# Kernel tuning notes

Measured on AMD Instinct MI355X. Metric: run time of the kernel, lower is better.

The kernel has to match this reference:

```python
import jax, jax.numpy as jnp
import numpy as np

INPUT_DIM = 1024
HIDDEN_DIM = 2048
LATENT_DIM = 256
NUM_EMBEDDINGS = 8192
COMMITMENT_COST = 0.25
BATCH = 16384


def setup_inputs() -> dict:
    key = jax.random.key(0)
    ks = jax.random.split(key, 10)
    def lin(k, fan_in, fan_out):
        # torch nn.Linear default init: U(-1/sqrt(fan_in), 1/sqrt(fan_in))
        bound = 1.0 / np.sqrt(fan_in)
        kw, kb = jax.random.split(k)
        W = jax.random.uniform(kw, (fan_in, fan_out), jnp.float32, -bound, bound)
        b = jax.random.uniform(kb, (fan_out,), jnp.float32, -bound, bound)
        return W, b
    enc_w1, enc_b1 = lin(ks[0], INPUT_DIM, HIDDEN_DIM)
    enc_w2, enc_b2 = lin(ks[1], HIDDEN_DIM, LATENT_DIM)
    dec_w1, dec_b1 = lin(ks[2], LATENT_DIM, HIDDEN_DIM)
    dec_w2, dec_b2 = lin(ks[3], HIDDEN_DIM, INPUT_DIM)
    # codebook init: U(-1/K, 1/K)
    codebook = jax.random.uniform(ks[4], (NUM_EMBEDDINGS, LATENT_DIM), jnp.float32,
                                  -1.0 / NUM_EMBEDDINGS, 1.0 / NUM_EMBEDDINGS)
    x = jax.random.uniform(ks[5], (BATCH, INPUT_DIM), jnp.float32)
    return {"x": x,
            "enc_w1": enc_w1, "enc_b1": enc_b1, "enc_w2": enc_w2, "enc_b2": enc_b2,
            "codebook": codebook,
            "dec_w1": dec_w1, "dec_b1": dec_b1, "dec_w2": dec_w2, "dec_b2": dec_b2}


def reference(x, enc_w1, enc_b1, enc_w2, enc_b2, codebook,
              dec_w1, dec_b1, dec_w2, dec_b2):
    # Encoder: relu(x W1 + b1) W2 + b2 -> z [N, latent]
    h = jax.nn.relu(x @ enc_w1 + enc_b1)
    z = h @ enc_w2 + enc_b2

    # Vector quantizer: squared-L2 distances to codebook [N, K]
    d = (jnp.sum(z * z, axis=1, keepdims=True)
         + jnp.sum(codebook * codebook, axis=1)
         - 2.0 * (z @ codebook.T))
    idx = jnp.argmin(d, axis=1)          # [N] int
    z_q = codebook[idx]                   # gather [N, latent]

    vq_loss = jnp.mean((jax.lax.stop_gradient(z_q) - z) ** 2)
    commit_loss = COMMITMENT_COST * jnp.mean((z_q - jax.lax.stop_gradient(z)) ** 2)
    loss = vq_loss + commit_loss

    # straight-through estimator
    z_q = z + jax.lax.stop_gradient(z_q - z)

    # Decoder: sigmoid(relu(z_q Wd1 + bd1) Wd2 + bd2)
    hd = jax.nn.relu(z_q @ dec_w1 + dec_b1)
    x_recon = jax.nn.sigmoid(hd @ dec_w2 + dec_b2)
    return (x_recon, loss)
```

## Files before the change

### kernel.cpp

```cpp
#include <hip/hip_runtime.h>
#include <math.h>

typedef unsigned short u16;
typedef __bf16 bf16x8 __attribute__((ext_vector_type(8)));
typedef float  f32x4  __attribute__((ext_vector_type(4)));

constexpr int B_  = 16384;
constexpr int DIN = 1024;
constexpr int DH  = 2048;
constexpr int DL  = 256;
constexpr int NE  = 8192;

__device__ __forceinline__ u16 f2bf(float f) {
    union { float f; unsigned u; } v; v.f = f;
    unsigned r = v.u + 0x7fffu + ((v.u >> 16) & 1u);
    return (u16)(r >> 16);
}
__device__ __forceinline__ float bf2f(u16 h) {
    union { unsigned u; float f; } v; v.u = ((unsigned)h) << 16;
    return v.f;
}

#define GLD16(gp, lp)                                                  \
    __builtin_amdgcn_global_load_lds(                                  \
        (__attribute__((address_space(1))) void*)(gp),                 \
        (__attribute__((address_space(3))) void*)(lp), 16, 0, 0)

#define SCHED0() __builtin_amdgcn_sched_barrier(0)
#define BARRIER() do { SCHED0(); __builtin_amdgcn_s_barrier(); SCHED0(); } while (0)
#define WAITV0() asm volatile("s_waitcnt vmcnt(0)" ::: "memory")
#define WAITV3() asm volatile("s_waitcnt vmcnt(3)" ::: "memory")

__device__ __forceinline__ void dev_cast(const float* __restrict__ in,
                                         u16* __restrict__ out, long blk)
{
    const size_t i = ((size_t)blk * 256 + threadIdx.x) * 4;
    float4 v = *(const float4*)(in + i);
    ushort4 o;
    o.x = f2bf(v.x); o.y = f2bf(v.y); o.z = f2bf(v.z); o.w = f2bf(v.w);
    *(ushort4*)(out + i) = o;
}

__device__ __forceinline__ void dev_transpose(const float* __restrict__ in,
                                              u16* __restrict__ out,
                                              int R, int C, long bx, long by,
                                              float (*t)[33])
{
    const int tx = threadIdx.x & 31, ty = threadIdx.x >> 5;
#pragma unroll
    for (int p = 0; p < 4; ++p)
        t[ty + p * 8][tx] = in[(by * 32 + ty + p * 8) * (long)C + bx * 32 + tx];
    __syncthreads();
#pragma unroll
    for (int p = 0; p < 4; ++p)
        out[(bx * 32 + ty + p * 8) * (long)R + by * 32 + tx] = f2bf(t[tx][ty + p * 8]);
}

__global__ __launch_bounds__(256)
void prep_fused(const float* __restrict__ x,   u16* __restrict__ x_bf,
                const float* __restrict__ cb,  u16* __restrict__ cb_bf,
                const float* __restrict__ ew1, u16* __restrict__ w1t,
                const float* __restrict__ ew2, u16* __restrict__ w2t,
                const float* __restrict__ dw1, u16* __restrict__ wd1t,
                const float* __restrict__ dw2, u16* __restrict__ wd2t,
                float* __restrict__ cn2)
{
    __shared__ float t[32][33];
    const long b = blockIdx.x;

    if (b < 16384) {
        dev_cast(x, x_bf, b);
    } else if (b < 18432) {
        dev_cast(cb, cb_bf, b - 16384);
    } else if (b < 20480) {
        const long r = b - 18432;
        dev_transpose(ew1, w1t, DIN, DH, r % 64, r / 64, t);
    } else if (b < 20992) {
        const long r = b - 20480;
        dev_transpose(ew2, w2t, DH, DL, r % 8, r / 8, t);
    } else if (b < 21504) {
        const long r = b - 20992;
        dev_transpose(dw1, wd1t, DL, DH, r % 64, r / 64, t);
    } else if (b < 23552) {
        const long r = b - 21504;
        dev_transpose(dw2, wd2t, DH, DIN, r % 32, r / 32, t);
    } else {
        const long r = b - 23552;
        const int code = (int)((r * 256 + threadIdx.x) >> 6);
        const int lane = threadIdx.x & 63;
        float4 v = *(const float4*)(cb + (long)code * DL + lane * 4);
        float s = fmaf(v.x, v.x, fmaf(v.y, v.y, fmaf(v.z, v.z, v.w * v.w)));
#pragma unroll
        for (int off = 32; off; off >>= 1) s += __shfl_down(s, off);
        if (lane == 0) cn2[code] = 0.5f * s;
    }
}

template <int EPI>
__global__ __launch_bounds__(512, 4)
void gemm_big_bf16(const u16* __restrict__ A, const u16* __restrict__ Bt,
                   const float* __restrict__ bias, void* __restrict__ Cout,
                   int M, int N, int K)
{
    __shared__ __align__(16) u16 As[3 * 8192];
    __shared__ __align__(16) u16 Bs[3 * 4096];

    const int tid = threadIdx.x;
    const int w = tid >> 6, l = tid & 63;
    const int wm = w >> 1, wn = w & 1;

    const int nbx   = N >> 7;
    const int nwg   = (M >> 8) * nbx;
    const int chunk = nwg >> 3;
    const int wg    = ((int)blockIdx.x & 7) * chunk + ((int)blockIdx.x >> 3);
    const long by   = wg / nbx;
    const long bx   = wg % nbx;

    const int lr  = l >> 2;
    const int lsw = (l & 3) ^ ((l >> 3) & 3);
    const int lg  = l >> 4, lm = l & 15;
    const int sx  = (lm >> 1) & 3;

    const u16* Abase = A  + (size_t)(by * 256) * K;
    const u16* Bbase = Bt + (size_t)(bx * 128) * K;

    f32x4 acc[4][4] = {};

    auto stage = [&](int k0, int b) {
        u16* dA = As + b * 8192;
        u16* dB = Bs + b * 4096;
#pragma unroll
        for (int i = 0; i < 2; ++i) {
            const int seg = w * 2 + i;
            GLD16(Abase + (size_t)(seg * 16 + lr) * K + k0 + lsw * 8,
                  dA + seg * 512);
        }
        GLD16(Bbase + (size_t)(w * 16 + lr) * K + k0 + lsw * 8,
              dB + w * 512);
    };

    const int NT = K >> 5;
    stage(0, 0);
    stage(32, 1);

    int cur = 0, pre = 2;
    for (int t = 0; t < NT; ++t) {
        if (t + 1 < NT) { WAITV3(); } else { WAITV0(); }
        BARRIER();
        if (t + 2 < NT) stage((t + 2) << 5, pre);

        const u16* as = As + cur * 8192;
        const u16* bs = Bs + cur * 4096;
        bf16x8 af[4], bfr[4];
#pragma unroll
        for (int m = 0; m < 4; ++m) {
            const int R = wm * 64 + m * 16 + lm;
            af[m] = *(const bf16x8*)&as[R * 32 + ((lg ^ sx) * 8)];
        }
#pragma unroll
        for (int n = 0; n < 4; ++n) {
            const int R = wn * 64 + n * 16 + lm;
            bfr[n] = *(const bf16x8*)&bs[R * 32 + ((lg ^ sx) * 8)];
        }
#pragma unroll
        for (int m = 0; m < 4; ++m)
#pragma unroll
            for (int n = 0; n < 4; ++n)
                acc[m][n] = __builtin_amdgcn_mfma_f32_16x16x32_bf16(
                    af[m], bfr[n], acc[m][n], 0, 0, 0);

        cur = (cur == 2) ? 0 : cur + 1;
        pre = (pre == 2) ? 0 : pre + 1;
    }

#pragma unroll
    for (int n = 0; n < 4; ++n) {
        const long col = bx * 128 + wn * 64 + n * 16 + lm;
        const float bb = bias[col];
#pragma unroll
        for (int m = 0; m < 4; ++m) {
#pragma unroll
            for (int j = 0; j < 4; ++j) {
                const long row = by * 256 + wm * 64 + m * 16 + lg * 4 + j;
                float e = acc[m][n][j] + bb;
                if (EPI == 1) e = fmaxf(e, 0.f);
                if (EPI == 2) {
                    e = 1.f / (1.f + expf(-e));
                    ((float*)Cout)[row * (long)N + col] = e;
                } else {
                    ((u16*)Cout)[row * (long)N + col] = f2bf(e);
                }
            }
        }
    }
}

template <int EPI>
__global__ __launch_bounds__(256, 4)
void gemm_64_bf16(const u16* __restrict__ A, const u16* __restrict__ Bt,
                  const float* __restrict__ bias, void* __restrict__ Cout,
                  int M, int N, int K)
{
    __shared__ __align__(16) u16 As[3 * 2048];
    __shared__ __align__(16) u16 Bs[3 * 4096];

    const int tid = threadIdx.x;
    const int w = tid >> 6, l = tid & 63;

    const int nbx   = N >> 7;
    const int nwg   = (M >> 6) * nbx;
    const int chunk = nwg >> 3;
    const int wg    = ((int)blockIdx.x & 7) * chunk + ((int)blockIdx.x >> 3);
    const long by   = wg / nbx;
    const long bx   = wg % nbx;

    const int lr  = l >> 2;
    const int lsw = (l & 3) ^ ((l >> 3) & 3);
    const int lg  = l >> 4, lm = l & 15;
    const int sx  = (lm >> 1) & 3;

    const u16* Abase = A  + (size_t)(by * 64) * K;
    const u16* Bbase = Bt + (size_t)(bx * 128) * K;

    f32x4 acc[4][2] = {};

    auto stage = [&](int k0, int b) {
        u16* dA = As + b * 2048;
        u16* dB = Bs + b * 4096;
        GLD16(Abase + (size_t)(w * 16 + lr) * K + k0 + lsw * 8, dA + w * 512);
#pragma unroll
        for (int i = 0; i < 2; ++i) {
            const int seg = w * 2 + i;
            GLD16(Bbase + (size_t)(seg * 16 + lr) * K + k0 + lsw * 8,
                  dB + seg * 512);
        }
    };

    const int NT = K >> 5;
    stage(0, 0);
    stage(32, 1);

    int cur = 0, pre = 2;
    for (int t = 0; t < NT; ++t) {
        if (t + 1 < NT) { WAITV3(); } else { WAITV0(); }
        BARRIER();
        if (t + 2 < NT) stage((t + 2) << 5, pre);

        const u16* as = As + cur * 2048;
        const u16* bs = Bs + cur * 4096;
        bf16x8 af[4], bfr[2];
#pragma unroll
        for (int m = 0; m < 4; ++m)
            af[m] = *(const bf16x8*)&as[(m * 16 + lm) * 32 + ((lg ^ sx) * 8)];
#pragma unroll
        for (int n = 0; n < 2; ++n) {
            const int R = w * 32 + n * 16 + lm;
            bfr[n] = *(const bf16x8*)&bs[R * 32 + ((lg ^ sx) * 8)];
        }
#pragma unroll
        for (int m = 0; m < 4; ++m)
#pragma unroll
            for (int n = 0; n < 2; ++n)
                acc[m][n] = __builtin_amdgcn_mfma_f32_16x16x32_bf16(
                    af[m], bfr[n], acc[m][n], 0, 0, 0);

        cur = (cur == 2) ? 0 : cur + 1;
        pre = (pre == 2) ? 0 : pre + 1;
    }

#pragma unroll
    for (int n = 0; n < 2; ++n) {
        const long col = bx * 128 + w * 32 + n * 16 + lm;
        const float bb = bias[col];
#pragma unroll
        for (int m = 0; m < 4; ++m) {
#pragma unroll
            for (int j = 0; j < 4; ++j) {
                const long row = by * 64 + m * 16 + lg * 4 + j;
                float e = acc[m][n][j] + bb;
                if (EPI == 2) {
                    e = 1.f / (1.f + expf(-e));
                    ((float*)Cout)[row * (long)N + col] = e;
                } else {
                    ((u16*)Cout)[row * (long)N + col] = f2bf(e);
                }
            }
        }
    }
}

__global__ __launch_bounds__(256, 2)
void vq_score2(const u16* __restrict__ z, const u16* __restrict__ cbt,
               const float* __restrict__ cn2,
               float* __restrict__ val8, int* __restrict__ idx8)
{
    __shared__ __align__(16) u16 lds[32768];

    const int tid = threadIdx.x;
    const int w = tid >> 6, l = tid & 63;
    const int rq = blockIdx.x >> 3;
    const int q  = blockIdx.x & 7;

    const int st_row8 = tid >> 5;
    const int st_s    = (tid & 31) ^ st_row8;
    const int lg = l >> 4, lm = l & 15;
    const int swz_x = l & 7;

    bf16x8 af[4][8];
    const long zbase_row = (long)rq * 256;
#pragma unroll
    for (int h = 0; h < 2; ++h) {
#pragma unroll
        for (int i = 0; i < 16; ++i) {
            const int row = i * 8 + st_row8;
            const u16* g = z + (zbase_row + h * 128 + row) * DL + st_s * 8;
            GLD16(g, lds + ((size_t)i * 256 + w * 64) * 8);
        }
        __syncthreads();
        if ((w >> 1) == h) {
            const int lrow0 = (w & 1) * 64;
#pragma unroll
            for (int m = 0; m < 4; ++m) {
                const int lrow = lrow0 + m * 16 + lm;
#pragma unroll
                for (int kg = 0; kg < 8; ++kg) {
                    const int s = (kg * 4 + lg) ^ swz_x;
                    af[m][kg] = *(const bf16x8*)&lds[lrow * 256 + s * 8];
                }
            }
        }
        __syncthreads();
    }

    const int code00 = q * (NE / 8);

    float bestv[16];
    int   besti[16];
#pragma unroll
    for (int k = 0; k < 16; ++k) { bestv[k] = 1e30f; besti[k] = 0; }

    auto stage_tile = [&](int t) {
        const int b = t & 1;
#pragma unroll
        for (int i = 0; i < 8; ++i) {
            const int c = i * 8 + st_row8;
            const u16* g = cbt + (size_t)(code00 + t * 64 + c) * DL + st_s * 8;
            GLD16(g, lds + ((size_t)b * 16384 + ((size_t)i * 256 + w * 64) * 8));
        }
    };

    stage_tile(0);
    __syncthreads();

    for (int t = 0; t < 16; ++t) {
        if (t < 15) stage_tile(t + 1);
        const u16* buf = lds + (size_t)(t & 1) * 16384;

#pragma unroll
        for (int n = 0; n < 4; ++n) {
            const int code_g = code00 + t * 64 + n * 16 + lm;
            const float cn2v = cn2[code_g];
            bf16x8 bfr[8];
#pragma unroll
            for (int kg = 0; kg < 8; ++kg) {
                const int lrow = n * 16 + lm;
                const int s = (kg * 4 + lg) ^ swz_x;
                bfr[kg] = *(const bf16x8*)&buf[lrow * 256 + s * 8];
            }
            f32x4 acc[4] = {};
#pragma unroll
            for (int kg = 0; kg < 8; ++kg)
#pragma unroll
                for (int m = 0; m < 4; ++m)
                    acc[m] = __builtin_amdgcn_mfma_f32_16x16x32_bf16(
                        af[m][kg], bfr[kg], acc[m], 0, 0, 0);
#pragma unroll
            for (int m = 0; m < 4; ++m)
#pragma unroll
                for (int j = 0; j < 4; ++j) {
                    const float s = cn2v - acc[m][j];
                    const int k16 = m * 4 + j;
                    if (s < bestv[k16]) { bestv[k16] = s; besti[k16] = code_g; }
                }
        }
        __syncthreads();
    }

#pragma unroll
    for (int off = 1; off < 16; off <<= 1) {
#pragma unroll
        for (int k = 0; k < 16; ++k) {
            const float ov = __shfl_xor(bestv[k], off);
            const int   oi = __shfl_xor(besti[k], off);
            if (ov < bestv[k] || (ov == bestv[k] && oi < besti[k])) {
                bestv[k] = ov; besti[k] = oi;
            }
        }
    }
    if (lm == 0) {
#pragma unroll
        for (int m = 0; m < 4; ++m)
#pragma unroll
            for (int j = 0; j < 4; ++j) {
                const long row = zbase_row + w * 64 + m * 16 + lg * 4 + j;
                val8[(size_t)q * B_ + row] = bestv[m * 4 + j];
                idx8[(size_t)q * B_ + row] = besti[m * 4 + j];
            }
    }
}

__global__ __launch_bounds__(256)
void vq_select2(const float* __restrict__ val8, const int* __restrict__ idx8,
                const u16* __restrict__ z, const float* __restrict__ cb,
                int* __restrict__ idxf, float* __restrict__ partial)
{
    __shared__ int   s_idx[256];
    __shared__ float s_red[4];
    const int tid = threadIdx.x;
    const long row = (long)blockIdx.x * 256 + tid;

    float bv = val8[row];
    int   bi = idx8[row];
#pragma unroll
    for (int qq = 1; qq < 8; ++qq) {
        const float v = val8[(size_t)qq * B_ + row];
        const int   i = idx8[(size_t)qq * B_ + row];
        if (v < bv || (v == bv && i < bi)) { bv = v; bi = i; }
    }
    s_idx[tid] = bi;
    idxf[row]  = bi;
    __syncthreads();

    float ls = 0.f;
    const int sub = tid & 7;
#pragma unroll
    for (int pass = 0; pass < 8; ++pass) {
        const int rl = pass * 32 + (tid >> 3);
        const int gi = s_idx[rl];
        const long rg = (long)blockIdx.x * 256 + rl;
#pragma unroll
        for (int tt = 0; tt < 8; ++tt) {
            const int d = sub * 4 + tt * 32;
            float4 c4 = *(const float4*)(cb + (long)gi * DL + d);
            ushort4 zu = *(const ushort4*)(z + rg * DL + d);
            const float dx = c4.x - bf2f(zu.x), dy = c4.y - bf2f(zu.y);
            const float dz = c4.z - bf2f(zu.z), dw = c4.w - bf2f(zu.w);
            ls += dx * dx + dy * dy + dz * dz + dw * dw;
        }
    }
#pragma unroll
    for (int off = 32; off; off >>= 1) ls += __shfl_down(ls, off);
    if ((tid & 63) == 0) s_red[tid >> 6] = ls;
    __syncthreads();
    if (tid == 0)
        partial[blockIdx.x] = s_red[0] + s_red[1] + s_red[2] + s_red[3];
}

__global__ __launch_bounds__(256)
void loss_finalize(const float* __restrict__ partial, float* __restrict__ out)
{
    __shared__ float s_red[4];
    const int tid = threadIdx.x;
    float s = (tid < 64) ? partial[tid] : 0.f;
#pragma unroll
    for (int off = 32; off; off >>= 1) s += __shfl_down(s, off);
    if ((tid & 63) == 0) s_red[tid >> 6] = s;
    __syncthreads();
    if (tid == 0)
        out[0] = 1.25f * (s_red[0] + s_red[1] + s_red[2] + s_red[3])
                 / (float)((long)B_ * DL);
}

__global__ __launch_bounds__(256)
void gather_rows(const float* __restrict__ Xcode, const int* __restrict__ idxf,
                 float* __restrict__ out)
{
    const int tid  = threadIdx.x;
    const int lane = tid & 63;
    const long row = (long)blockIdx.x * 4 + (tid >> 6);
    const long gi  = idxf[row];
    const float* src = Xcode + gi * DIN;
    float*       dst = out + row * DIN;
#pragma unroll
    for (int t = 0; t < 4; ++t) {
        const int d = lane * 4 + t * 256;
        *(float4*)(dst + d) = *(const float4*)(src + d);
    }
}

extern "C" void kernel_launch(void* const* d_in, const int* in_sizes, int n_in,
                              void* d_out, int out_size, void* d_ws, size_t ws_size,
                              hipStream_t stream)
{
    const float* x   = (const float*)d_in[0];
    const float* ew1 = (const float*)d_in[1];
    const float* eb1 = (const float*)d_in[2];
    const float* ew2 = (const float*)d_in[3];
    const float* eb2 = (const float*)d_in[4];
    const float* cbk = (const float*)d_in[5];
    const float* dw1 = (const float*)d_in[6];
    const float* db1 = (const float*)d_in[7];
    const float* dw2 = (const float*)d_in[8];
    const float* db2 = (const float*)d_in[9];
    float* out = (float*)d_out;

    char* p = (char*)d_ws;
    auto alloc = [&](size_t bytes) {
        char* r = p; p += (bytes + 255) & ~(size_t)255; return r;
    };
    u16*   x_bf  = (u16*)alloc((size_t)B_ * DIN * 2);
    u16*   h_bf  = (u16*)alloc((size_t)B_ * DH * 2);
    u16*   z_bf  = (u16*)alloc((size_t)B_ * DL * 2);
    u16*   cb_bf = (u16*)alloc((size_t)NE * DL * 2);
    u16*   w1t   = (u16*)alloc((size_t)DH * DIN * 2);
    u16*   w2t   = (u16*)alloc((size_t)DL * DH * 2);
    u16*   wd1t  = (u16*)alloc((size_t)DH * DL * 2);
    u16*   wd2t  = (u16*)alloc((size_t)DIN * DH * 2);
    float* Xcode = (float*)alloc((size_t)NE * DIN * 4);
    float* cn2   = (float*)alloc((size_t)NE * 4);
    float* val8  = (float*)alloc((size_t)8 * B_ * 4);
    int*   idx8  = (int*)alloc((size_t)8 * B_ * 4);
    int*   idxf  = (int*)alloc((size_t)B_ * 4);
    float* part  = (float*)alloc(64 * 4);

    prep_fused<<<25600, 256, 0, stream>>>(x, x_bf, cbk, cb_bf,
                                          ew1, w1t, ew2, w2t,
                                          dw1, wd1t, dw2, wd2t, cn2);

    gemm_big_bf16<1><<<(B_ / 256) * (DH / 128), 512, 0, stream>>>(
        x_bf, w1t, eb1, h_bf, B_, DH, DIN);
    gemm_64_bf16<0><<<(B_ / 64) * (DL / 128), 256, 0, stream>>>(
        h_bf, w2t, eb2, z_bf, B_, DL, DH);

    vq_score2<<<512, 256, 0, stream>>>(z_bf, cb_bf, cn2, val8, idx8);
    vq_select2<<<B_ / 256, 256, 0, stream>>>(val8, idx8, z_bf, cbk, idxf, part);
    loss_finalize<<<1, 256, 0, stream>>>(part, out + (size_t)B_ * DIN);

    gemm_big_bf16<1><<<(NE / 256) * (DH / 128), 512, 0, stream>>>(
        cb_bf, wd1t, db1, h_bf, NE, DH, DL);
    gemm_64_bf16<2><<<(NE / 64) * (DIN / 128), 256, 0, stream>>>(
        h_bf, wd2t, db2, Xcode, NE, DIN, DH);
    gather_rows<<<B_ / 4, 256, 0, stream>>>(Xcode, idxf, out);
}
```

Measured before the change: 300.3 us.

## Fuse encoder second GEMM with codebook decoder first GEMM in one launch

Merges the small-N encoder GEMM (z = h·W2) and the codebook decoder first layer into a single kernel that dispatches on block index, so the 512-block encoder GEMM no longer leaves CUs idle. The decoder first layer moves from the large 256x128 tile kernel to the 64x128 tile core, and its output reuses the dead x_bf buffer. The epilogue mode becomes a runtime argument, and the decoder second GEMM is launched before the VQ kernels.

```diff
diff --git a/kernel.cpp b/kernel.cpp
--- a/kernel.cpp
+++ b/kernel.cpp
@@ -184,7 +184,94 @@
                 const long row = by * 256 + wm * 64 + m * 16 + lg * 4 + j;
                 float e = acc[m][n][j] + bb;
                 if (EPI == 1) e = fmaxf(e, 0.f);
-                if (EPI == 2) {
+                ((u16*)Cout)[row * (long)N + col] = f2bf(e);
+            }
+        }
+    }
+}
+
+__device__ __forceinline__ void gemm64_core(
+    const u16* __restrict__ A, const u16* __restrict__ Bt,
+    const float* __restrict__ bias, void* __restrict__ Cout,
+    int M, int N, int K, int epi, int bid,
+    u16* __restrict__ As, u16* __restrict__ Bs)
+{
+    const int tid = threadIdx.x;
+    const int w = tid >> 6, l = tid & 63;
+
+    const int nbx   = N >> 7;
+    const int nwg   = (M >> 6) * nbx;
+    const int chunk = nwg >> 3;
+    const int wg    = (bid & 7) * chunk + (bid >> 3);
+    const long by   = wg / nbx;
+    const long bx   = wg % nbx;
+
+    const int lr  = l >> 2;
+    const int lsw = (l & 3) ^ ((l >> 3) & 3);
+    const int lg  = l >> 4, lm = l & 15;
+    const int sx  = (lm >> 1) & 3;
+
+    const u16* Abase = A  + (size_t)(by * 64) * K;
+    const u16* Bbase = Bt + (size_t)(bx * 128) * K;
+
+    f32x4 acc[4][2] = {};
+
+    auto stage = [&](int k0, int b) {
+        u16* dA = As + b * 2048;
+        u16* dB = Bs + b * 4096;
+        GLD16(Abase + (size_t)(w * 16 + lr) * K + k0 + lsw * 8, dA + w * 512);
+#pragma unroll
+        for (int i = 0; i < 2; ++i) {
+            const int seg = w * 2 + i;
+            GLD16(Bbase + (size_t)(seg * 16 + lr) * K + k0 + lsw * 8,
+                  dB + seg * 512);
+        }
+    };
+
+    const int NT = K >> 5;
+    stage(0, 0);
+    stage(32, 1);
+
+    int cur = 0, pre = 2;
+    for (int t = 0; t < NT; ++t) {
+        if (t + 1 < NT) { WAITV3(); } else { WAITV0(); }
+        BARRIER();
+        if (t + 2 < NT) stage((t + 2) << 5, pre);
+
+        const u16* as = As + cur * 2048;
+        const u16* bs = Bs + cur * 4096;
+        bf16x8 af[4], bfr[2];
+#pragma unroll
+        for (int m = 0; m < 4; ++m)
+            af[m] = *(const bf16x8*)&as[(m * 16 + lm) * 32 + ((lg ^ sx) * 8)];
+#pragma unroll
+        for (int n = 0; n < 2; ++n) {
+            const int R = w * 32 + n * 16 + lm;
+            bfr[n] = *(const bf16x8*)&bs[R * 32 + ((lg ^ sx) * 8)];
+        }
+#pragma unroll
+        for (int m = 0; m < 4; ++m)
+#pragma unroll
+            for (int n = 0; n < 2; ++n)
+                acc[m][n] = __builtin_amdgcn_mfma_f32_16x16x32_bf16(
+                    af[m], bfr[n], acc[m][n], 0, 0, 0);
+
+        cur = (cur == 2) ? 0 : cur + 1;
+        pre = (pre == 2) ? 0 : pre + 1;
+    }
+
+#pragma unroll
+    for (int n = 0; n < 2; ++n) {
+        const long col = bx * 128 + w * 32 + n * 16 + lm;
+        const float bb = bias[col];
+#pragma unroll
+        for (int m = 0; m < 4; ++m) {
+#pragma unroll
+            for (int j = 0; j < 4; ++j) {
+                const long row = by * 64 + m * 16 + lg * 4 + j;
+                float e = acc[m][n][j] + bb;
+                if (epi == 1) e = fmaxf(e, 0.f);
+                if (epi == 2) {
                     e = 1.f / (1.f + expf(-e));
                     ((float*)Cout)[row * (long)N + col] = e;
                 } else {
@@ -195,98 +282,28 @@
     }
 }
 
-template <int EPI>
 __global__ __launch_bounds__(256, 4)
-void gemm_64_bf16(const u16* __restrict__ A, const u16* __restrict__ Bt,
-                  const float* __restrict__ bias, void* __restrict__ Cout,
-                  int M, int N, int K)
+void gemm2_dec1_fused(const u16* __restrict__ h,  const u16* __restrict__ w2t,
+                      const float* __restrict__ eb2, u16* __restrict__ z,
+                      const u16* __restrict__ cb, const u16* __restrict__ wd1t,
+                      const float* __restrict__ db1, u16* __restrict__ hcode)
 {
     __shared__ __align__(16) u16 As[3 * 2048];
     __shared__ __align__(16) u16 Bs[3 * 4096];
-
-    const int tid = threadIdx.x;
-    const int w = tid >> 6, l = tid & 63;
-
-    const int nbx   = N >> 7;
-    const int nwg   = (M >> 6) * nbx;
-    const int chunk = nwg >> 3;
-    const int wg    = ((int)blockIdx.x & 7) * chunk + ((int)blockIdx.x >> 3);
-    const long by   = wg / nbx;
-    const long bx   = wg % nbx;
-
-    const int lr  = l >> 2;
-    const int lsw = (l & 3) ^ ((l >> 3) & 3);
-    const int lg  = l >> 4, lm = l & 15;
-    const int sx  = (lm >> 1) & 3;
-
-    const u16* Abase = A  + (size_t)(by * 64) * K;
-    const u16* Bbase = Bt + (size_t)(bx * 128) * K;
-
-    f32x4 acc[4][2] = {};
-
-    auto stage = [&](int k0, int b) {
-        u16* dA = As + b * 2048;
-        u16* dB = Bs + b * 4096;
-        GLD16(Abase + (size_t)(w * 16 + lr) * K + k0 + lsw * 8, dA + w * 512);
-#pragma unroll
-        for (int i = 0; i < 2; ++i) {
-            const int seg = w * 2 + i;
-            GLD16(Bbase + (size_t)(seg * 16 + lr) * K + k0 + lsw * 8,
-                  dB + seg * 512);
-        }
-    };
-
-    const int NT = K >> 5;
-    stage(0, 0);
-    stage(32, 1);
-
-    int cur = 0, pre = 2;
-    for (int t = 0; t < NT; ++t) {
-        if (t + 1 < NT) { WAITV3(); } else { WAITV0(); }
-        BARRIER();
-        if (t + 2 < NT) stage((t + 2) << 5, pre);
-
-        const u16* as = As + cur * 2048;
-        const u16* bs = Bs + cur * 4096;
-        bf16x8 af[4], bfr[2];
-#pragma unroll
-        for (int m = 0; m < 4; ++m)
-            af[m] = *(const bf16x8*)&as[(m * 16 + lm) * 32 + ((lg ^ sx) * 8)];
-#pragma unroll
-        for (int n = 0; n < 2; ++n) {
-            const int R = w * 32 + n * 16 + lm;
-            bfr[n] = *(const bf16x8*)&bs[R * 32 + ((lg ^ sx) * 8)];
-        }
-#pragma unroll
-        for (int m = 0; m < 4; ++m)
-#pragma unroll
-            for (int n = 0; n < 2; ++n)
-                acc[m][n] = __builtin_amdgcn_mfma_f32_16x16x32_bf16(
-                    af[m], bfr[n], acc[m][n], 0, 0, 0);
-
-        cur = (cur == 2) ? 0 : cur + 1;
-        pre = (pre == 2) ? 0 : pre + 1;
-    }
-
-#pragma unroll
-    for (int n = 0; n < 2; ++n) {
-        const long col = bx * 128 + w * 32 + n * 16 + lm;
-        const float bb = bias[col];
-#pragma unroll
-        for (int m = 0; m < 4; ++m) {
-#pragma unroll
-            for (int j = 0; j < 4; ++j) {
-                const long row = by * 64 + m * 16 + lg * 4 + j;
-                float e = acc[m][n][j] + bb;
-                if (EPI == 2) {
-                    e = 1.f / (1.f + expf(-e));
-                    ((float*)Cout)[row * (long)N + col] = e;
-                } else {
-                    ((u16*)Cout)[row * (long)N + col] = f2bf(e);
-                }
-            }
-        }
-    }
+    const int b = (int)blockIdx.x;
+    if (b < 512)
+        gemm64_core(h, w2t, eb2, z, B_, DL, DH, 0, b, As, Bs);
+    else
+        gemm64_core(cb, wd1t, db1, hcode, NE, DH, DL, 1, b - 512, As, Bs);
+}
+
+__global__ __launch_bounds__(256, 4)
+void gemm_dec2(const u16* __restrict__ hcode, const u16* __restrict__ wd2t,
+               const float* __restrict__ db2, float* __restrict__ Xcode)
+{
+    __shared__ __align__(16) u16 As[3 * 2048];
+    __shared__ __align__(16) u16 Bs[3 * 4096];
+    gemm64_core(hcode, wd2t, db2, Xcode, NE, DIN, DH, 2, (int)blockIdx.x, As, Bs);
 }
 
 __global__ __launch_bounds__(256, 2)
@@ -523,22 +540,24 @@
     int*   idxf  = (int*)alloc((size_t)B_ * 4);
     float* part  = (float*)alloc(64 * 4);
 
+    u16* hcode = x_bf;
+
     prep_fused<<<25600, 256, 0, stream>>>(x, x_bf, cbk, cb_bf,
                                           ew1, w1t, ew2, w2t,
                                           dw1, wd1t, dw2, wd2t, cn2);
 
     gemm_big_bf16<1><<<(B_ / 256) * (DH / 128), 512, 0, stream>>>(
         x_bf, w1t, eb1, h_bf, B_, DH, DIN);
-    gemm_64_bf16<0><<<(B_ / 64) * (DL / 128), 256, 0, stream>>>(
-        h_bf, w2t, eb2, z_bf, B_, DL, DH);
+
+    gemm2_dec1_fused<<<2560, 256, 0, stream>>>(h_bf, w2t, eb2, z_bf,
+                                               cb_bf, wd1t, db1, hcode);
+
+    gemm_dec2<<<(NE / 64) * (DIN / 128), 256, 0, stream>>>(
+        hcode, wd2t, db2, Xcode);
 
     vq_score2<<<512, 256, 0, stream>>>(z_bf, cb_bf, cn2, val8, idx8);
     vq_select2<<<B_ / 256, 256, 0, stream>>>(val8, idx8, z_bf, cbk, idxf, part);
     loss_finalize<<<1, 256, 0, stream>>>(part, out + (size_t)B_ * DIN);
 
-    gemm_big_bf16<1><<<(NE / 256) * (DH / 128), 512, 0, stream>>>(
-        cb_bf, wd1t, db1, h_bf, NE, DH, DL);
-    gemm_64_bf16<2><<<(NE / 64) * (DIN / 128), 256, 0, stream>>>(
-        h_bf, wd2t, db2, Xcode, NE, DIN, DH);
     gather_rows<<<B_ / 4, 256, 0, stream>>>(Xcode, idxf, out);
 }
```

New measurement: 294.0 us. -2.1%, faster.
